# Performance work log

Measured on AMD Instinct MI355X. Metric: run time of the kernel, lower is better.

Reference implementation:

```python
import jax, jax.numpy as jnp
import numpy as np

D_FEAT = 6
HIDDEN = 64
NEG_SLOPE = 0.01  # torch LeakyReLU default


def gru_layer(x, Wih, Whh, bih, bhh):
    # x: [N, T, D] -> outputs [N, T, H], PyTorch GRU gate math (r,z,n order)
    N = x.shape[0]
    H = Whh.shape[1]
    def step(h, xt):
        gi = xt @ Wih.T + bih          # [N, 3H]
        gh = h @ Whh.T + bhh           # [N, 3H]
        i_r, i_z, i_n = jnp.split(gi, 3, axis=-1)
        h_r, h_z, h_n = jnp.split(gh, 3, axis=-1)
        r = jax.nn.sigmoid(i_r + h_r)
        z = jax.nn.sigmoid(i_z + h_z)
        n = jnp.tanh(i_n + r * h_n)
        h_new = (1.0 - z) * n + z * h
        return h_new, h_new
    h0 = jnp.zeros((N, H), x.dtype)
    _, hs = jax.lax.scan(step, h0, jnp.swapaxes(x, 0, 1))  # hs: [T, N, H]
    return jnp.swapaxes(hs, 0, 1)


def setup_inputs() -> dict:
    key = jax.random.key(0)
    ks = jax.random.split(key, 16)
    N, T, D, H, R = 2048, 60, D_FEAT, HIDDEN, 20
    x = jax.random.normal(ks[0], (N, D * T), dtype=jnp.float32)
    vals = jax.random.uniform(ks[1], (N, N, R), dtype=jnp.float32)
    keep = jax.random.uniform(ks[2], (N, N, R), dtype=jnp.float32) < 0.3
    relation_matrix = vals * keep.astype(jnp.float32)
    s = 1.0 / np.sqrt(H)
    def u(k, shape):
        return jax.random.uniform(k, shape, dtype=jnp.float32, minval=-s, maxval=s)
    inp = {
        "x": x,
        "relation_matrix": relation_matrix,
        "Wih0": u(ks[3], (3 * H, D)),
        "Whh0": u(ks[4], (3 * H, H)),
        "bih0": u(ks[5], (3 * H,)),
        "bhh0": u(ks[6], (3 * H,)),
        "Wih1": u(ks[7], (3 * H, H)),
        "Whh1": u(ks[8], (3 * H, H)),
        "bih1": u(ks[9], (3 * H,)),
        "bhh1": u(ks[10], (3 * H,)),
        "W": jax.random.normal(ks[11], (2 * H + R, 1), dtype=jnp.float32) * 0.1,
        "b": jnp.zeros((1,), dtype=jnp.float32),
        "fc_w": u(ks[12], (1, H)),
        "fc_b": jnp.zeros((1,), dtype=jnp.float32),
    }
    return inp


def reference(x, relation_matrix, Wih0, Whh0, bih0, bhh0, Wih1, Whh1, bih1, bhh1, W, b, fc_w, fc_b):
    N = x.shape[0]
    H = HIDDEN
    R = relation_matrix.shape[2]
    # [N, d_feat*T] -> [N, T, d_feat]
    xs = jnp.transpose(x.reshape(N, D_FEAT, -1), (0, 2, 1))
    h = gru_layer(xs, Wih0, Whh0, bih0, bhh0)
    h = gru_layer(h, Wih1, Whh1, bih1, bhh1)
    x_hidden = h[:, -1, :]  # [N, H]
    # decompose concat @ W:  W = [W1 (ei part); W2 (hidden part); W3 (relation part)]
    W1 = W[:H, 0]
    W2 = W[H:2 * H, 0]
    W3 = W[2 * H:, 0]
    ai = x_hidden @ W1          # [N] contribution of row i
    aj = x_hidden @ W2          # [N] contribution of col j
    ar = jnp.einsum('ijr,r->ij', relation_matrix, W3)  # [N, N]
    weight = ai[:, None] + aj[None, :] + ar + b[0]
    weight = jnp.where(weight >= 0, weight, NEG_SLOPE * weight)  # leaky_relu
    mask = (jnp.sum(relation_matrix, axis=2) != 0).astype(x_hidden.dtype)
    valid_weight = mask * weight
    valid_weight = jax.nn.softmax(valid_weight, axis=1)
    hidden = valid_weight @ x_hidden  # [N, H]
    pred_all = ((hidden + x_hidden) @ fc_w.T + fc_b).squeeze(-1)  # [N]
    return pred_all
```

## Files before the change

kernel.cpp:

```cpp
#include <hip/hip_runtime.h>
#include <cstddef>

typedef __attribute__((ext_vector_type(8))) short short8;
typedef __attribute__((ext_vector_type(4))) float f32x4;

#define MFMA16(a, b, c) __builtin_amdgcn_mfma_f32_16x16x32_bf16((a), (b), (c), 0, 0, 0)

__device__ __forceinline__ unsigned short f2bf(float f) {
    unsigned u = __float_as_uint(f);
    u = (u + 0x7fffu + ((u >> 16) & 1u)) >> 16;
    return (unsigned short)u;
}
__device__ __forceinline__ float bf2f(unsigned short s) {
    return __uint_as_float(((unsigned)s) << 16);
}
__device__ __forceinline__ float sigm(float v) { return 1.f / (1.f + __expf(-v)); }
__device__ __forceinline__ float tanh_(float v) {
    float a = fabsf(v);
    float e = __expf(-2.f * a);
    float t = (1.f - e) / (1.f + e);
    return v < 0.f ? -t : t;
}

__device__ __forceinline__ void lds_order_fence() {
    asm volatile("" ::: "memory");
    __builtin_amdgcn_sched_barrier(0);
}

__launch_bounds__(768, 3)
__global__ void mega_kernel(const float* __restrict__ x,
                            const float* __restrict__ Wih0, const float* __restrict__ Whh0,
                            const float* __restrict__ bih0, const float* __restrict__ bhh0,
                            const float* __restrict__ Wih1, const float* __restrict__ Whh1,
                            const float* __restrict__ bih1, const float* __restrict__ bhh1,
                            const float* __restrict__ rel, const float* __restrict__ W,
                            float* __restrict__ xhid, float* __restrict__ arw,
                            unsigned long long* __restrict__ maskw) {
    __shared__ __align__(16) unsigned char smem[79744];

    const int tid  = threadIdx.x;
    const int lane = tid & 63;

    if (blockIdx.x >= 256) {
        const int bid = blockIdx.x - 256;
        const int wv  = tid >> 6;
        const int gw  = bid * 12 + wv;
        float* b = (float*)smem + wv * 1280;

        float w3[20];
#pragma unroll
        for (int e = 0; e < 20; ++e) w3[e] = W[128 + e];

        f32x4 A0, A1, A2, A3, A4, B0, B1, B2, B3, B4;

#define REL_ISSUE(tsk, R0, R1, R2, R3, R4)                                       \
    {                                                                            \
        const float* gp = rel + (size_t)(tsk) * 1280 + lane * 4;                 \
        R0 = *(const f32x4*)(gp);                                                \
        R1 = *(const f32x4*)(gp + 256);                                          \
        R2 = *(const f32x4*)(gp + 512);                                          \
        R3 = *(const f32x4*)(gp + 768);                                          \
        R4 = *(const f32x4*)(gp + 1024);                                         \
    }

#define REL_CONSUME(tsk, R0, R1, R2, R3, R4)                                     \
    {                                                                            \
        *(f32x4*)&b[0    + lane * 4] = R0;                                       \
        *(f32x4*)&b[256  + lane * 4] = R1;                                       \
        *(f32x4*)&b[512  + lane * 4] = R2;                                       \
        *(f32x4*)&b[768  + lane * 4] = R3;                                       \
        *(f32x4*)&b[1024 + lane * 4] = R4;                                       \
        lds_order_fence();                              \
        float arv = 0.f, ms = 0.f;                                               \
        _Pragma("unroll")                                                        \
        for (int e = 0; e < 5; ++e) {                                            \
            const f32x4 v = *(const f32x4*)&b[lane * 20 + e * 4];                \
            arv += v[0] * w3[e * 4] + v[1] * w3[e * 4 + 1]                       \
                 + v[2] * w3[e * 4 + 2] + v[3] * w3[e * 4 + 3];                  \
            ms  += v[0] + v[1] + v[2] + v[3];                                    \
        }                                                                        \
        lds_order_fence();             \
        arw[(size_t)(tsk) * 64 + lane] = arv;                                    \
        const unsigned long long bal = __ballot(ms != 0.f);                      \
        if (lane == 0) maskw[tsk] = bal;                                         \
    }

        int t = gw, k = 0;
        REL_ISSUE(t, A0, A1, A2, A3, A4);
        while (t < 65536) {
            const int tn = t + 9216;
            if ((k & 1) == 0) {
                if (tn < 65536) REL_ISSUE(tn, B0, B1, B2, B3, B4);
                REL_CONSUME(t, A0, A1, A2, A3, A4);
            } else {
                if (tn < 65536) REL_ISSUE(tn, A0, A1, A2, A3, A4);
                REL_CONSUME(t, B0, B1, B2, B3, B4);
            }
            t = tn; ++k;
        }
#undef REL_ISSUE
#undef REL_CONSUME
        return;
    }

    typedef unsigned short ush;
    ush (*h0h)[1024] = (ush (*)[1024])(smem);
    ush (*h0l)[1024] = (ush (*)[1024])(smem + 4096);
    ush (*h1h)[1024] = (ush (*)[1024])(smem + 8192);
    ush (*h1l)[1024] = (ush (*)[1024])(smem + 12288);
    float (*P1)[16][195] = (float (*)[16][195])(smem + 16384);
    short8* axbuf = (short8*)(smem + 41344);

    const int grp  = tid >> 8;
    const int gw_  = (tid >> 6) & 3;
    const int c    = lane & 15;
    const int q    = lane >> 4;
    const int jj   = gw_ * 16 + c;

    for (int i = tid; i < 1024; i += 768) {
        h0h[0][i] = 0; h0l[0][i] = 0; h1h[0][i] = 0; h1l[0][i] = 0;
    }
    {
        const float* xb = x + (size_t)blockIdx.x * 8 * 360;
        for (int f = tid; f < 1920; f += 768) {
            const int t = f >> 5, s = (f >> 2) & 7, qq = f & 3;
            unsigned short Hh[6], Ll[6];
#pragma unroll
            for (int d = 0; d < 6; ++d) {
                const float v = xb[s * 360 + d * 60 + t];
                Hh[d] = f2bf(v); Ll[d] = f2bf(v - bf2f(Hh[d]));
            }
            short8 fr;
#pragma unroll
            for (int e = 0; e < 8; ++e) {
                const int k = qq * 8 + e;
                unsigned short u = 0;
                if (k < 6) u = Hh[k];
                else if (k < 12) u = Ll[k - 6];
                else if (k < 18) u = Hh[k - 12];
                fr[e] = (short)u;
            }
            axbuf[t * 40 + s * 5 + qq] = fr;
        }
    }

    const int ka    = q * 8;
    const int swzA0 = c * 64 + (ka ^ ((c & 7) << 3));
    const int swzA1 = c * 64 + ((32 + ka) ^ ((c & 7) << 3));

    __syncthreads();

    if (grp == 0) {
        short8 Bhh[3][2], Bhl[3][2], Bc[3];
#pragma unroll
        for (int g = 0; g < 3; ++g) {
            const int o = g * 64 + jj;
#pragma unroll
            for (int kt = 0; kt < 2; ++kt) {
                const int k0 = kt * 32 + q * 8;
#pragma unroll
                for (int e = 0; e < 8; ++e) {
                    const float v = Whh0[o * 64 + k0 + e];
                    const unsigned short hi = f2bf(v);
                    Bhh[g][kt][e] = (short)hi; Bhl[g][kt][e] = (short)f2bf(v - bf2f(hi));
                }
            }
#pragma unroll
            for (int e = 0; e < 8; ++e) {
                const int ks = q * 8 + e;
                unsigned short bv = 0;
                if (ks < 6)       bv = f2bf(Wih0[o * 6 + ks]);
                else if (ks < 12) bv = f2bf(Wih0[o * 6 + ks - 6]);
                else if (ks < 18) {
                    const float v = Wih0[o * 6 + ks - 12];
                    const unsigned short hi = f2bf(v);
                    bv = f2bf(v - bf2f(hi));
                }
                Bc[g][e] = (short)bv;
            }
        }
        const float br = bih0[jj] + bhh0[jj];
        const float bz = bih0[64 + jj] + bhh0[64 + jj];
        const float bi = bih0[128 + jj];
        const float bh = bhh0[128 + jj];
        float hreg[4] = {0.f, 0.f, 0.f, 0.f};

        for (int it = 0; it < 62; ++it) {
            if (it < 60) {
                const int par = it & 1;
                const short8 ah0 = *(const short8*)&h0h[par][swzA0];
                const short8 ah1 = *(const short8*)&h0h[par][swzA1];
                const short8 al0 = *(const short8*)&h0l[par][swzA0];
                const short8 al1 = *(const short8*)&h0l[par][swzA1];
                const short8 ax  = axbuf[it * 40 + (c & 7) * 5 + q];

                f32x4 accr = {br, br, br, br};
                f32x4 accz = {bz, bz, bz, bz};
                f32x4 acci = {bi, bi, bi, bi};
                f32x4 acch = {bh, bh, bh, bh};

                accr = MFMA16(ah0, Bhh[0][0], accr); accr = MFMA16(ah1, Bhh[0][1], accr);
                accr = MFMA16(al0, Bhh[0][0], accr); accr = MFMA16(al1, Bhh[0][1], accr);
                accr = MFMA16(ah0, Bhl[0][0], accr); accr = MFMA16(ah1, Bhl[0][1], accr);
                accr = MFMA16(ax, Bc[0], accr);

                accz = MFMA16(ah0, Bhh[1][0], accz); accz = MFMA16(ah1, Bhh[1][1], accz);
                accz = MFMA16(al0, Bhh[1][0], accz); accz = MFMA16(al1, Bhh[1][1], accz);
                accz = MFMA16(ah0, Bhl[1][0], accz); accz = MFMA16(ah1, Bhl[1][1], accz);
                accz = MFMA16(ax, Bc[1], accz);

                acci = MFMA16(ax, Bc[2], acci);

                acch = MFMA16(ah0, Bhh[2][0], acch); acch = MFMA16(ah1, Bhh[2][1], acch);
                acch = MFMA16(al0, Bhh[2][0], acch); acch = MFMA16(al1, Bhh[2][1], acch);
                acch = MFMA16(ah0, Bhl[2][0], acch); acch = MFMA16(ah1, Bhl[2][1], acch);

#pragma unroll
                for (int i2 = 0; i2 < 4; ++i2) {
                    const float rr = sigm(accr[i2]);
                    const float zz = sigm(accz[i2]);
                    const float nn = tanh_(acci[i2] + rr * acch[i2]);
                    const float hv = (1.f - zz) * nn + zz * hreg[i2];
                    hreg[i2] = hv;
                    const int r  = q * 4 + i2;
                    const int ix = r * 64 + (jj ^ ((r & 7) << 3));
                    const unsigned short hi = f2bf(hv);
                    h0h[par ^ 1][ix] = hi;
                    h0l[par ^ 1][ix] = f2bf(hv - bf2f(hi));
                }
            }
            __syncthreads();
        }
    } else if (grp == 1) {
        short8 Bih[3][2], Bil[3][2];
#pragma unroll
        for (int g = 0; g < 3; ++g) {
            const int o = g * 64 + jj;
#pragma unroll
            for (int kt = 0; kt < 2; ++kt) {
                const int k0 = kt * 32 + q * 8;
#pragma unroll
                for (int e = 0; e < 8; ++e) {
                    const float v = Wih1[o * 64 + k0 + e];
                    const unsigned short hi = f2bf(v);
                    Bih[g][kt][e] = (short)hi; Bil[g][kt][e] = (short)f2bf(v - bf2f(hi));
                }
            }
        }
        const float br = bih1[jj] + bhh1[jj];
        const float bz = bih1[64 + jj] + bhh1[64 + jj];
        const float bi = bih1[128 + jj];

        for (int it = 0; it < 62; ++it) {
            if (it >= 1 && it < 61) {
                const int par = it & 1;
                const short8 gh0 = *(const short8*)&h0h[par][swzA0];
                const short8 gh1 = *(const short8*)&h0h[par][swzA1];
                const short8 gl0 = *(const short8*)&h0l[par][swzA0];
                const short8 gl1 = *(const short8*)&h0l[par][swzA1];

                f32x4 ar = {br, br, br, br};
                f32x4 az = {bz, bz, bz, bz};
                f32x4 an = {bi, bi, bi, bi};

                ar = MFMA16(gh0, Bih[0][0], ar); ar = MFMA16(gh1, Bih[0][1], ar);
                ar = MFMA16(gl0, Bih[0][0], ar); ar = MFMA16(gl1, Bih[0][1], ar);
                ar = MFMA16(gh0, Bil[0][0], ar); ar = MFMA16(gh1, Bil[0][1], ar);

                az = MFMA16(gh0, Bih[1][0], az); az = MFMA16(gh1, Bih[1][1], az);
                az = MFMA16(gl0, Bih[1][0], az); az = MFMA16(gl1, Bih[1][1], az);
                az = MFMA16(gh0, Bil[1][0], az); az = MFMA16(gh1, Bil[1][1], az);

                an = MFMA16(gh0, Bih[2][0], an); an = MFMA16(gh1, Bih[2][1], an);
                an = MFMA16(gl0, Bih[2][0], an); an = MFMA16(gl1, Bih[2][1], an);
                an = MFMA16(gh0, Bil[2][0], an); an = MFMA16(gh1, Bil[2][1], an);

#pragma unroll
                for (int i2 = 0; i2 < 4; ++i2) {
                    const int r = q * 4 + i2;
                    P1[par][r][jj]       = ar[i2];
                    P1[par][r][64 + jj]  = az[i2];
                    P1[par][r][128 + jj] = an[i2];
                }
            }
            __syncthreads();
        }
    } else {
        short8 Bhh[3][2], Bhl[3][2];
#pragma unroll
        for (int g = 0; g < 3; ++g) {
            const int o = g * 64 + jj;
#pragma unroll
            for (int kt = 0; kt < 2; ++kt) {
                const int k0 = kt * 32 + q * 8;
#pragma unroll
                for (int e = 0; e < 8; ++e) {
                    const float v = Whh1[o * 64 + k0 + e];
                    const unsigned short hi = f2bf(v);
                    Bhh[g][kt][e] = (short)hi; Bhl[g][kt][e] = (short)f2bf(v - bf2f(hi));
                }
            }
        }
        const float bh = bhh1[128 + jj];
        float hreg[4] = {0.f, 0.f, 0.f, 0.f};

        for (int it = 0; it < 62; ++it) {
            if (it >= 2) {
                const int par = it & 1;
                const short8 hh0 = *(const short8*)&h1h[par][swzA0];
                const short8 hh1_ = *(const short8*)&h1h[par][swzA1];
                const short8 hl0 = *(const short8*)&h1l[par][swzA0];
                const short8 hl1_ = *(const short8*)&h1l[par][swzA1];

                float p1r[4], p1z[4], p1n[4];
#pragma unroll
                for (int i2 = 0; i2 < 4; ++i2) {
                    const int r = q * 4 + i2;
                    p1r[i2] = P1[par ^ 1][r][jj];
                    p1z[i2] = P1[par ^ 1][r][64 + jj];
                    p1n[i2] = P1[par ^ 1][r][128 + jj];
                }

                f32x4 ar  = {p1r[0], p1r[1], p1r[2], p1r[3]};
                f32x4 az  = {p1z[0], p1z[1], p1z[2], p1z[3]};
                f32x4 ahn = {bh, bh, bh, bh};

                ar = MFMA16(hh0, Bhh[0][0], ar); ar = MFMA16(hh1_, Bhh[0][1], ar);
                ar = MFMA16(hl0, Bhh[0][0], ar); ar = MFMA16(hl1_, Bhh[0][1], ar);
                ar = MFMA16(hh0, Bhl[0][0], ar); ar = MFMA16(hh1_, Bhl[0][1], ar);

                az = MFMA16(hh0, Bhh[1][0], az); az = MFMA16(hh1_, Bhh[1][1], az);
                az = MFMA16(hl0, Bhh[1][0], az); az = MFMA16(hl1_, Bhh[1][1], az);
                az = MFMA16(hh0, Bhl[1][0], az); az = MFMA16(hh1_, Bhl[1][1], az);

                ahn = MFMA16(hh0, Bhh[2][0], ahn); ahn = MFMA16(hh1_, Bhh[2][1], ahn);
                ahn = MFMA16(hl0, Bhh[2][0], ahn); ahn = MFMA16(hl1_, Bhh[2][1], ahn);
                ahn = MFMA16(hh0, Bhl[2][0], ahn); ahn = MFMA16(hh1_, Bhl[2][1], ahn);

#pragma unroll
                for (int i2 = 0; i2 < 4; ++i2) {
                    const float rr = sigm(ar[i2]);
                    const float zz = sigm(az[i2]);
                    const float nn = tanh_(p1n[i2] + rr * ahn[i2]);
                    const float hv = (1.f - zz) * nn + zz * hreg[i2];
                    hreg[i2] = hv;
                    const int r  = q * 4 + i2;
                    const int ix = r * 64 + (jj ^ ((r & 7) << 3));
                    const unsigned short hi = f2bf(hv);
                    h1h[par ^ 1][ix] = hi;
                    h1l[par ^ 1][ix] = f2bf(hv - bf2f(hi));
                    if (it == 61 && q < 2)
                        xhid[((size_t)blockIdx.x * 8 + r) * 64 + jj] = hv;
                }
            }
            __syncthreads();
        }
    }
}

__global__ void aij_kernel(const float* __restrict__ xh, const float* __restrict__ W,
                           float* __restrict__ ai, float* __restrict__ aj) {
    const int n = blockIdx.x * 256 + threadIdx.x;
    const float* row = xh + (size_t)n * 64;
    float a1 = 0.f, a2 = 0.f;
#pragma unroll
    for (int k = 0; k < 64; k += 4) {
        const f32x4 v = *(const f32x4*)(row + k);
#pragma unroll
        for (int u = 0; u < 4; ++u) {
            a1 += v[u] * W[k + u];
            a2 += v[u] * W[64 + k + u];
        }
    }
    ai[n] = a1;
    aj[n] = a2;
}

__launch_bounds__(1024, 2)
__global__ void finish_kernel(const float* __restrict__ arw,
                              const unsigned long long* __restrict__ maskw,
                              const float* __restrict__ xh, const float* __restrict__ ai,
                              const float* __restrict__ aj, const float* __restrict__ bptr,
                              const float* __restrict__ fcw, const float* __restrict__ fcb,
                              float* __restrict__ out) {
    __shared__ __align__(16) float sc[8][2056];
    __shared__ __align__(16) float hidpart[16][8][64];
    __shared__ float redm[8][2], reds[8][2], rinv_s[8];

    const int tid = threadIdx.x;
    const int i0  = blockIdx.x * 8;

    float aiv[8];
#pragma unroll
    for (int il = 0; il < 8; ++il) aiv[il] = ai[i0 + il];
    const float bb = bptr[0];

#pragma unroll
    for (int jc = 0; jc < 2; ++jc) {
        const int j = tid + jc * 1024;
        const float ajv = aj[j];
#pragma unroll
        for (int il = 0; il < 8; ++il) {
            const float s = arw[(size_t)(i0 + il) * 2048 + j];
            const unsigned long long mw = maskw[(size_t)(i0 + il) * 32 + (j >> 6)];
            float wvv = aiv[il] + ajv + s + bb;
            wvv = (wvv >= 0.f) ? wvv : 0.01f * wvv;
            sc[il][j] = ((mw >> (j & 63)) & 1ull) ? wvv : 0.f;
        }
    }
    __syncthreads();

    const int row = tid >> 7;
    const int c7  = tid & 127;
    const int wh  = (tid >> 6) & 1;

    float mx = -1e30f;
#pragma unroll
    for (int m = 0; m < 16; ++m) mx = fmaxf(mx, sc[row][c7 + 128 * m]);
#pragma unroll
    for (int d = 1; d < 64; d <<= 1) mx = fmaxf(mx, __shfl_xor(mx, d, 64));
    if ((tid & 63) == 0) redm[row][wh] = mx;
    __syncthreads();
    mx = fmaxf(redm[row][0], redm[row][1]);

    float sm = 0.f;
#pragma unroll
    for (int m = 0; m < 16; ++m) {
        const int k = c7 + 128 * m;
        const float e = __expf(sc[row][k] - mx);
        sc[row][k] = e;
        sm += e;
    }
#pragma unroll
    for (int d = 1; d < 64; d <<= 1) sm += __shfl_xor(sm, d, 64);
    if ((tid & 63) == 0) reds[row][wh] = sm;
    __syncthreads();
    if ((tid & 127) == 0) rinv_s[row] = 1.f / (reds[row][0] + reds[row][1]);

    const int col   = tid & 63;
    const int strip = tid >> 6;
    const int k0s   = strip * 128;

    float acc[8] = {0.f, 0.f, 0.f, 0.f, 0.f, 0.f, 0.f, 0.f};
    for (int k = 0; k < 128; k += 4) {
        const float v0 = xh[(size_t)(k0s + k) * 64 + col];
        const float v1 = xh[(size_t)(k0s + k + 1) * 64 + col];
        const float v2 = xh[(size_t)(k0s + k + 2) * 64 + col];
        const float v3 = xh[(size_t)(k0s + k + 3) * 64 + col];
#pragma unroll
        for (int il = 0; il < 8; ++il) {
            const f32x4 e = *(const f32x4*)&sc[il][k0s + k];
            acc[il] += e[0] * v0 + e[1] * v1 + e[2] * v2 + e[3] * v3;
        }
    }
#pragma unroll
    for (int il = 0; il < 8; ++il) hidpart[strip][il][col] = acc[il];
    __syncthreads();

    if (tid < 512) {
        const int r2 = tid >> 6;
        const int cl = tid & 63;
        float hsum = 0.f;
#pragma unroll
        for (int s = 0; s < 16; ++s) hsum += hidpart[s][r2][cl];
        const float h = hsum * rinv_s[r2] + xh[(size_t)(i0 + r2) * 64 + cl];
        float p = h * fcw[cl];
#pragma unroll
        for (int d = 1; d < 64; d <<= 1) p += __shfl_xor(p, d, 64);
        if (cl == 0) out[i0 + r2] = p + fcb[0];
    }
}

extern "C" void kernel_launch(void* const* d_in, const int* in_sizes, int n_in,
                              void* d_out, int out_size, void* d_ws, size_t ws_size,
                              hipStream_t stream) {
    const float* x    = (const float*)d_in[0];
    const float* rel  = (const float*)d_in[1];
    const float* Wih0 = (const float*)d_in[2];
    const float* Whh0 = (const float*)d_in[3];
    const float* bih0 = (const float*)d_in[4];
    const float* bhh0 = (const float*)d_in[5];
    const float* Wih1 = (const float*)d_in[6];
    const float* Whh1 = (const float*)d_in[7];
    const float* bih1 = (const float*)d_in[8];
    const float* bhh1 = (const float*)d_in[9];
    const float* W    = (const float*)d_in[10];
    const float* b    = (const float*)d_in[11];
    const float* fcw  = (const float*)d_in[12];
    const float* fcb  = (const float*)d_in[13];
    float* out = (float*)d_out;

    float* xh = (float*)d_ws;
    float* ai = xh + 131072;
    float* aj = ai + 2048;
    float* arw = aj + 2048;
    unsigned long long* maskw = (unsigned long long*)(arw + 4194304);

    mega_kernel<<<1024, 768, 0, stream>>>(x, Wih0, Whh0, bih0, bhh0,
                                          Wih1, Whh1, bih1, bhh1,
                                          rel, W, xh, arw, maskw);
    aij_kernel<<<8, 256, 0, stream>>>(xh, W, ai, aj);
    finish_kernel<<<256, 1024, 0, stream>>>(arw, maskw, xh, ai, aj, b, fcw, fcb, out);
}
```

Before: 188.0 us.

## Reduce relation tensor with wave shuffles instead of LDS transpose, pack mask as 12-bit words

```diff
diff --git a/kernel.cpp b/kernel.cpp
--- a/kernel.cpp
+++ b/kernel.cpp
@@ -20,11 +20,6 @@
     float e = __expf(-2.f * a);
     float t = (1.f - e) / (1.f + e);
     return v < 0.f ? -t : t;
-}
-
-__device__ __forceinline__ void lds_order_fence() {
-    asm volatile("" ::: "memory");
-    __builtin_amdgcn_sched_barrier(0);
 }
 
 __launch_bounds__(768, 3)
@@ -35,74 +30,62 @@
                             const float* __restrict__ bih1, const float* __restrict__ bhh1,
                             const float* __restrict__ rel, const float* __restrict__ W,
                             float* __restrict__ xhid, float* __restrict__ arw,
-                            unsigned long long* __restrict__ maskw) {
+                            unsigned short* __restrict__ maskw16) {
     __shared__ __align__(16) unsigned char smem[79744];
 
     const int tid  = threadIdx.x;
     const int lane = tid & 63;
 
     if (blockIdx.x >= 256) {
-        const int bid = blockIdx.x - 256;
-        const int wv  = tid >> 6;
-        const int gw  = bid * 12 + wv;
-        float* b = (float*)smem + wv * 1280;
-
-        float w3[20];
-#pragma unroll
-        for (int e = 0; e < 20; ++e) w3[e] = W[128 + e];
-
-        f32x4 A0, A1, A2, A3, A4, B0, B1, B2, B3, B4;
-
-#define REL_ISSUE(tsk, R0, R1, R2, R3, R4)                                       \
+        __builtin_amdgcn_s_setprio(0);
+        const int wv = tid >> 6;
+        const int gw = (blockIdx.x - 256) * 12 + wv;
+        const int g5 = lane / 5;
+        const int r5 = lane - 5 * g5;
+        float w4[4];
+#pragma unroll
+        for (int j = 0; j < 4; ++j) w4[j] = W[128 + r5 * 4 + j];
+
+#define LOADG(c, v)                                                              \
     {                                                                            \
-        const float* gp = rel + (size_t)(tsk) * 1280 + lane * 4;                 \
-        R0 = *(const f32x4*)(gp);                                                \
-        R1 = *(const f32x4*)(gp + 256);                                          \
-        R2 = *(const f32x4*)(gp + 512);                                          \
-        R3 = *(const f32x4*)(gp + 768);                                          \
-        R4 = *(const f32x4*)(gp + 1024);                                         \
-    }
-
-#define REL_CONSUME(tsk, R0, R1, R2, R3, R4)                                     \
-    {                                                                            \
-        *(f32x4*)&b[0    + lane * 4] = R0;                                       \
-        *(f32x4*)&b[256  + lane * 4] = R1;                                       \
-        *(f32x4*)&b[512  + lane * 4] = R2;                                       \
-        *(f32x4*)&b[768  + lane * 4] = R3;                                       \
-        *(f32x4*)&b[1024 + lane * 4] = R4;                                       \
-        lds_order_fence();                              \
-        float arv = 0.f, ms = 0.f;                                               \
-        _Pragma("unroll")                                                        \
-        for (int e = 0; e < 5; ++e) {                                            \
-            const f32x4 v = *(const f32x4*)&b[lane * 20 + e * 4];                \
-            arv += v[0] * w3[e * 4] + v[1] * w3[e * 4 + 1]                       \
-                 + v[2] * w3[e * 4 + 2] + v[3] * w3[e * 4 + 3];                  \
-            ms  += v[0] + v[1] + v[2] + v[3];                                    \
-        }                                                                        \
-        lds_order_fence();             \
-        arw[(size_t)(tsk) * 64 + lane] = arv;                                    \
-        const unsigned long long bal = __ballot(ms != 0.f);                      \
-        if (lane == 0) maskw[tsk] = bal;                                         \
-    }
-
-        int t = gw, k = 0;
-        REL_ISSUE(t, A0, A1, A2, A3, A4);
-        while (t < 65536) {
-            const int tn = t + 9216;
-            if ((k & 1) == 0) {
-                if (tn < 65536) REL_ISSUE(tn, B0, B1, B2, B3, B4);
-                REL_CONSUME(t, A0, A1, A2, A3, A4);
-            } else {
-                if (tn < 65536) REL_ISSUE(tn, A0, A1, A2, A3, A4);
-                REL_CONSUME(t, B0, B1, B2, B3, B4);
-            }
-            t = tn; ++k;
-        }
-#undef REL_ISSUE
-#undef REL_CONSUME
+        const int off = (c) * 240 + lane * 4;                                    \
+        if (off < 83886080) v = *(const f32x4*)(rel + off);                      \
+        else { v[0] = 0.f; v[1] = 0.f; v[2] = 0.f; v[3] = 0.f; }                 \
+    }
+        f32x4 vc, vn;
+        LOADG(gw, vc);
+        for (int c = gw; c < 349526; c += 9216) {
+            if (c + 9216 < 349526) { LOADG(c + 9216, vn); }
+            else { vn[0] = 0.f; vn[1] = 0.f; vn[2] = 0.f; vn[3] = 0.f; }
+
+            const float pd = vc[0] * w4[0] + vc[1] * w4[1]
+                           + vc[2] * w4[2] + vc[3] * w4[3];
+            const float pm = vc[0] + vc[1] + vc[2] + vc[3];
+            float sd = pd + __shfl_down(pd, 1);
+            sd += __shfl_down(sd, 2);
+            sd += __shfl_down(pd, 4);
+            float sm = pm + __shfl_down(pm, 1);
+            sm += __shfl_down(sm, 2);
+            sm += __shfl_down(pm, 4);
+
+            const int p0 = c * 12 + g5;
+            if (r5 == 0 && g5 < 12 && p0 < 4194304) arw[p0] = sd;
+            const unsigned long long bal =
+                __ballot((r5 == 0) && (g5 < 12) && (sm != 0.f));
+            if (lane == 0) {
+                unsigned m16 = 0;
+#pragma unroll
+                for (int g = 0; g < 12; ++g)
+                    m16 |= ((unsigned)(bal >> (5 * g)) & 1u) << g;
+                maskw16[c] = (unsigned short)m16;
+            }
+            vc = vn;
+        }
+#undef LOADG
         return;
     }
 
+    __builtin_amdgcn_s_setprio(3);
     typedef unsigned short ush;
     ush (*h0h)[1024] = (ush (*)[1024])(smem);
     ush (*h0l)[1024] = (ush (*)[1024])(smem + 4096);
@@ -378,7 +361,7 @@
 
 __launch_bounds__(1024, 2)
 __global__ void finish_kernel(const float* __restrict__ arw,
-                              const unsigned long long* __restrict__ maskw,
+                              const unsigned short* __restrict__ maskw16,
                               const float* __restrict__ xh, const float* __restrict__ ai,
                               const float* __restrict__ aj, const float* __restrict__ bptr,
                               const float* __restrict__ fcw, const float* __restrict__ fcb,
@@ -401,11 +384,14 @@
         const float ajv = aj[j];
 #pragma unroll
         for (int il = 0; il < 8; ++il) {
-            const float s = arw[(size_t)(i0 + il) * 2048 + j];
-            const unsigned long long mw = maskw[(size_t)(i0 + il) * 32 + (j >> 6)];
+            const int p = (i0 + il) * 2048 + j;
+            const float s = arw[p];
+            const int cc = p / 12;
+            const int g  = p - cc * 12;
+            const unsigned m16 = maskw16[cc];
             float wvv = aiv[il] + ajv + s + bb;
             wvv = (wvv >= 0.f) ? wvv : 0.01f * wvv;
-            sc[il][j] = ((mw >> (j & 63)) & 1ull) ? wvv : 0.f;
+            sc[il][j] = ((m16 >> g) & 1u) ? wvv : 0.f;
         }
     }
     __syncthreads();
@@ -494,11 +480,11 @@
     float* ai = xh + 131072;
     float* aj = ai + 2048;
     float* arw = aj + 2048;
-    unsigned long long* maskw = (unsigned long long*)(arw + 4194304);
+    unsigned short* maskw16 = (unsigned short*)(arw + 4194304);
 
     mega_kernel<<<1024, 768, 0, stream>>>(x, Wih0, Whh0, bih0, bhh0,
                                           Wih1, Whh1, bih1, bhh1,
-                                          rel, W, xh, arw, maskw);
+                                          rel, W, xh, arw, maskw16);
     aij_kernel<<<8, 256, 0, stream>>>(xh, W, ai, aj);
-    finish_kernel<<<256, 1024, 0, stream>>>(arw, maskw, xh, ai, aj, b, fcw, fcb, out);
-}
+    finish_kernel<<<256, 1024, 0, stream>>>(arw, maskw16, xh, ai, aj, b, fcw, fcb, out);
+}
```

New measurement: 225.7 us. 20.1% more time.
